# Performance work log

Hardware: AMD Instinct MI355X
Metric: run time of the kernel (lower is better)

## Reference

```python
import jax, jax.numpy as jnp
import numpy as np

B, N, K, F, L, H, ZMAX = 16, 1024, 16, 128, 4, 128, 100


def setup_inputs() -> dict:
    key = jax.random.key(0)
    ks = jax.random.split(key, 12)
    cell = jnp.eye(3, dtype=jnp.float32)[None] * 8.0 + 0.05 * jax.random.normal(ks[0], (B, 3, 3), dtype=jnp.float32)
    x = jax.random.uniform(ks[1], (B, N, 3), dtype=jnp.float32)
    z = jax.random.randint(ks[2], (B, N), 0, ZMAX)
    struct_size = jnp.full((B,), N, dtype=jnp.int32)
    emb = 0.02 * jax.random.normal(ks[3], (ZMAX, F), dtype=jnp.float32)
    din = 2 * F + 1
    W1 = jax.random.normal(ks[4], (L, din, F), dtype=jnp.float32) / np.sqrt(din)
    b1 = jnp.zeros((L, F), dtype=jnp.float32)
    W2 = jax.random.normal(ks[5], (L, F, F), dtype=jnp.float32) / np.sqrt(F)
    b2 = jnp.zeros((L, F), dtype=jnp.float32)
    A1 = jax.random.normal(ks[6], (din, H), dtype=jnp.float32) / np.sqrt(din)
    a1 = jnp.zeros((H,), dtype=jnp.float32)
    A2 = jax.random.normal(ks[7], (H, 1), dtype=jnp.float32) / np.sqrt(H)
    a2 = jnp.zeros((1,), dtype=jnp.float32)
    return {"cell": cell, "x": x, "z": z, "struct_size": struct_size, "emb": emb,
            "W1": W1, "b1": b1, "W2": W2, "b2": b2, "A1": A1, "a1": a1, "A2": A2, "a2": a2}


def _periodic_knn(cell, frac, k):
    # frac: [B,N,3] fractional coords, cell: [B,3,3] lattice rows.
    b, n, _ = frac.shape
    g = jnp.arange(-1, 2, dtype=frac.dtype)
    shifts = jnp.stack(jnp.meshgrid(g, g, g, indexing="ij"), -1).reshape(-1, 3)  # [27,3]
    rel = frac[:, None, :, :] - frac[:, :, None, :]  # rel[b,i,j] = frac_j - frac_i, [B,N,N,3]

    def body(carry, si):
        bd2, bsi = carry
        s, i = si
        cart = jnp.einsum("bijd,bde->bije", rel + s, cell)
        d2 = jnp.sum(cart * cart, axis=-1)
        upd = d2 < bd2
        return (jnp.where(upd, d2, bd2), jnp.where(upd, i, bsi)), None

    init = (jnp.full((b, n, n), 1e30, dtype=frac.dtype), jnp.zeros((b, n, n), dtype=jnp.int32))
    (d2min, simin), _ = jax.lax.scan(body, init, (shifts, jnp.arange(27, dtype=jnp.int32)))
    eye = jnp.eye(n, dtype=bool)
    d2min = jnp.where(eye[None], 1e30, d2min)  # exclude self (zero-shift) edges
    _, idx = jax.lax.top_k(-d2min, k)  # [B,N,k] neighbor indices
    sid = jnp.take_along_axis(simin, idx, axis=2)  # best image shift per edge
    svec = shifts[sid]  # [B,N,k,3]
    frac_j = jax.vmap(lambda f, i: f[i])(frac, idx)  # [B,N,k,3]
    vec = jnp.einsum("bnkd,bde->bnke", frac_j - frac[:, :, None, :] + svec, cell)
    d = jnp.sqrt(jnp.maximum(jnp.sum(vec * vec, axis=-1), 1e-12))  # [B,N,k]
    return idx, vec, d


def _edge_feat(h, idx, d):
    hj = jax.vmap(lambda hb, ib: hb[ib])(h, idx)  # [B,N,k,F]
    hi = jnp.broadcast_to(h[:, :, None, :], hj.shape)
    return jnp.concatenate([hi, hj, d[..., None]], axis=-1)  # [B,N,k,2F+1]


def reference(cell, x, z, struct_size, emb, W1, b1, W2, b2, A1, a1, A2, a2):
    frac = jnp.mod(x, 1.0)
    idx, vec, d = _periodic_knn(cell, frac, K)
    h = emb[z]  # [B,N,F]
    for l in range(W1.shape[0]):
        feat = _edge_feat(h, idx, d)
        m = jax.nn.silu(feat @ W1[l] + b1[l]) @ W2[l] + b2[l]  # [B,N,k,F]
        h = h + jnp.mean(m, axis=2)
    feat = _edge_feat(h, idx, d)
    w = jax.nn.silu(feat @ A1 + a1) @ A2 + a2  # [B,N,k,1]
    delta_cart = jnp.sum(w * vec, axis=2)  # [B,N,3]
    delta_frac = jnp.einsum("bnd,bde->bne", delta_cart, jnp.linalg.inv(cell))
    return x + delta_frac
```

## Files before the change

### kernel.cpp

```cpp
#include <hip/hip_runtime.h>

#define B_ 16
#define N_ 1024
#define K_ 16
#define F_ 128
#define L_ 4
#define DIN_ 257

typedef __bf16 bf16x8 __attribute__((ext_vector_type(8)));
typedef float f32x4 __attribute__((ext_vector_type(4)));

__device__ __forceinline__ float silu_f(float x) {
    return x / (1.0f + __expf(-x));
}

__device__ __forceinline__ unsigned short f2bf_bits(float f) {
    unsigned u = __builtin_bit_cast(unsigned, f);
    return (unsigned short)((u + 0x7FFFu + ((u >> 16) & 1u)) >> 16);
}

__global__ __launch_bounds__(256) void k_embed(const int* __restrict__ z,
                                               const float* __restrict__ emb,
                                               float* __restrict__ h,
                                               unsigned short* __restrict__ hbf) {
    int t = blockIdx.x * 256 + threadIdx.x;
    int node = t >> 5;
    int f4 = (t & 31) << 2;
    if (node >= B_ * N_) return;
    int zi = z[node];
    float4 v = *reinterpret_cast<const float4*>(&emb[zi * F_ + f4]);
    *reinterpret_cast<float4*>(&h[node * F_ + f4]) = v;
    ushort4 pk;
    pk.x = f2bf_bits(v.x); pk.y = f2bf_bits(v.y);
    pk.z = f2bf_bits(v.z); pk.w = f2bf_bits(v.w);
    *reinterpret_cast<ushort4*>(&hbf[node * F_ + f4]) = pk;
}

__global__ __launch_bounds__(256) void k_wconv(const float* __restrict__ W1,
                                               const float* __restrict__ W2,
                                               const float* __restrict__ A1,
                                               unsigned short* __restrict__ Wt1,
                                               unsigned short* __restrict__ Wt2,
                                               unsigned short* __restrict__ At1) {
    int id = blockIdx.x * 256 + threadIdx.x;
    if (id < L_ * 256 * 128) {
        int k = id & 127, n = (id >> 7) & 255, l = id >> 15;
        float v = (n < 128) ? W1[(size_t)l * DIN_ * F_ + (size_t)k * F_ + n]
                            : W1[(size_t)l * DIN_ * F_ + (size_t)(128 + k) * F_ + (n - 128)];
        Wt1[id] = f2bf_bits(v);
        return;
    }
    id -= L_ * 256 * 128;
    if (id < L_ * 128 * 128) {
        int k = id & 127, n = (id >> 7) & 127, l = id >> 14;
        Wt2[id] = f2bf_bits(W2[(size_t)l * F_ * F_ + (size_t)k * F_ + n]);
        return;
    }
    id -= L_ * 128 * 128;
    if (id < 256 * 128) {
        int k = id & 127, n = id >> 7;
        float v = (n < 128) ? A1[(size_t)k * 128 + n]
                            : A1[(size_t)(128 + k) * 128 + (n - 128)];
        At1[id] = f2bf_bits(v);
    }
}

__global__ __launch_bounds__(256) void k_knn(const float* __restrict__ x,
                                             const float* __restrict__ cell,
                                             int* __restrict__ idx_o,
                                             float* __restrict__ vec_o,
                                             float* __restrict__ d_o) {
    __shared__ float fr[N_ * 3];
    int b = blockIdx.x >> 8;
    int ib = (blockIdx.x & 255) << 2;
    const float* xb = x + b * N_ * 3;
    for (int u = threadIdx.x; u < N_ * 3; u += 256) {
        float xv = xb[u];
        fr[u] = xv - floorf(xv);
    }
    __syncthreads();
    int wave = threadIdx.x >> 6;
    int lane = threadIdx.x & 63;
    int i = ib + wave;

    const float* cb = cell + b * 9;
    float c00 = cb[0], c01 = cb[1], c02 = cb[2];
    float c10 = cb[3], c11 = cb[4], c12 = cb[5];
    float c20 = cb[6], c21 = cb[7], c22 = cb[8];
    float fi0 = fr[i * 3 + 0], fi1 = fr[i * 3 + 1], fi2 = fr[i * 3 + 2];

    unsigned long long k[16];
#pragma unroll
    for (int t = 0; t < 16; ++t) {
        int j = t * 64 + lane;
        float r0 = fr[j * 3 + 0] - fi0;
        float r1 = fr[j * 3 + 1] - fi1;
        float r2 = fr[j * 3 + 2] - fi2;
        float s0f = (r0 > 0.f) ? -1.f : 0.f;
        float s1f = (r1 > 0.f) ? -1.f : 0.f;
        float s2f = (r2 > 0.f) ? -1.f : 0.f;
        int sid_base = ((r0 > 0.f) ? 0 : 9) + ((r1 > 0.f) ? 0 : 3) + ((r2 > 0.f) ? 0 : 1);
        float rx0 = r0 + s0f, rx1 = r0 + (s0f + 1.0f);
        float ry0 = r1 + s1f, ry1 = r1 + (s1f + 1.0f);
        float rz0 = r2 + s2f, rz1 = r2 + (s2f + 1.0f);
        float best = 3e38f;
        int bsid = 0;
#pragma unroll
        for (int cbo = 0; cbo < 8; ++cbo) {
            float rs0 = (cbo & 4) ? rx1 : rx0;
            float rs1 = (cbo & 2) ? ry1 : ry0;
            float rs2 = (cbo & 1) ? rz1 : rz0;
            float cx = fmaf(rs2, c20, fmaf(rs1, c10, rs0 * c00));
            float cy = fmaf(rs2, c21, fmaf(rs1, c11, rs0 * c01));
            float cz = fmaf(rs2, c22, fmaf(rs1, c12, rs0 * c02));
            float d2 = fmaf(cz, cz, fmaf(cy, cy, cx * cx));
            int sid = sid_base + ((cbo >> 2) & 1) * 9 + ((cbo >> 1) & 1) * 3 + (cbo & 1);
            if (d2 < best) { best = d2; bsid = sid; }
        }
        if (j == i) best = 3e38f;
        unsigned db = __builtin_bit_cast(unsigned, best);
        k[t] = ((unsigned long long)db << 32) | (unsigned)((j << 5) | bsid);
    }

#define CE_(a, b)                                              \
    {                                                          \
        unsigned long long x_ = k[a], y_ = k[b];               \
        bool s_ = y_ < x_;                                     \
        k[a] = s_ ? y_ : x_;                                   \
        k[b] = s_ ? x_ : y_;                                   \
    }
    CE_(0,1) CE_(2,3) CE_(4,5) CE_(6,7) CE_(8,9) CE_(10,11) CE_(12,13) CE_(14,15)
    CE_(0,2) CE_(1,3) CE_(4,6) CE_(5,7) CE_(8,10) CE_(9,11) CE_(12,14) CE_(13,15)
    CE_(1,2) CE_(5,6) CE_(9,10) CE_(13,14)
    CE_(0,4) CE_(1,5) CE_(2,6) CE_(3,7) CE_(8,12) CE_(9,13) CE_(10,14) CE_(11,15)
    CE_(2,4) CE_(3,5) CE_(10,12) CE_(11,13)
    CE_(1,2) CE_(3,4) CE_(5,6) CE_(9,10) CE_(11,12) CE_(13,14)
    CE_(0,8) CE_(1,9) CE_(2,10) CE_(3,11) CE_(4,12) CE_(5,13) CE_(6,14) CE_(7,15)
    CE_(4,8) CE_(5,9) CE_(6,10) CE_(7,11)
    CE_(2,4) CE_(3,5) CE_(6,8) CE_(7,9) CE_(10,12) CE_(11,13)
    CE_(1,2) CE_(3,4) CE_(5,6) CE_(7,8) CE_(9,10) CE_(11,12) CE_(13,14)
#undef CE_

    unsigned long long sel = 0;
    for (int r = 0; r < 16; ++r) {
        unsigned long long m = k[0];
#pragma unroll
        for (int off = 32; off >= 1; off >>= 1) {
            unsigned long long o = __shfl_xor(m, off);
            if (o < m) m = o;
        }
        if (k[0] == m) {
#pragma unroll
            for (int t = 0; t < 15; ++t) k[t] = k[t + 1];
            k[15] = ~0ull;
        }
        if (lane == r) sel = m;
    }

    if (lane < 16) {
        unsigned pk = (unsigned)sel;
        int j = pk >> 5, sid = pk & 31;
        int s0 = sid / 9 - 1, s1 = (sid / 3) % 3 - 1, s2 = sid % 3 - 1;
        float rs0 = (fr[j * 3 + 0] - fi0) + (float)s0;
        float rs1 = (fr[j * 3 + 1] - fi1) + (float)s1;
        float rs2 = (fr[j * 3 + 2] - fi2) + (float)s2;
        float vx = fmaf(rs2, c20, fmaf(rs1, c10, rs0 * c00));
        float vy = fmaf(rs2, c21, fmaf(rs1, c11, rs0 * c01));
        float vz = fmaf(rs2, c22, fmaf(rs1, c12, rs0 * c02));
        float d2 = fmaf(vz, vz, fmaf(vy, vy, vx * vx));
        float dd = sqrtf(fmaxf(d2, 1e-12f));
        int node = b * N_ + i;
        int eo = node * K_ + lane;
        idx_o[eo] = j;
        d_o[eo] = dd;
        vec_o[eo * 3 + 0] = vx;
        vec_o[eo * 3 + 1] = vy;
        vec_o[eo * 3 + 2] = vz;
    }
}

template <int LOG_NT>
__global__ __launch_bounds__(256) void k_wgemm(const unsigned short* __restrict__ A,
                                               const unsigned short* __restrict__ Bt,
                                               float* __restrict__ C, int ldc) {
    constexpr int NT = 1 << LOG_NT;
    int wave = threadIdx.x >> 6, lane = threadIdx.x & 63;
    int tile = blockIdx.x * 4 + wave;
    int mt = tile >> LOG_NT, nt = tile & (NT - 1);
    int fr16 = lane & 15, ko = lane >> 4;
    const unsigned short* Ap = A + (size_t)(mt * 32 + fr16) * 128 + ko * 8;
    const unsigned short* Bp = Bt + (size_t)(nt * 32 + fr16) * 128 + ko * 8;

    bf16x8 a0[4], a1[4], b0[4], b1[4];
#pragma unroll
    for (int ks = 0; ks < 4; ++ks) {
        a0[ks] = *reinterpret_cast<const bf16x8*>(Ap + ks * 32);
        a1[ks] = *reinterpret_cast<const bf16x8*>(Ap + 16 * 128 + ks * 32);
        b0[ks] = *reinterpret_cast<const bf16x8*>(Bp + ks * 32);
        b1[ks] = *reinterpret_cast<const bf16x8*>(Bp + 16 * 128 + ks * 32);
    }
    f32x4 acc00 = {0.f, 0.f, 0.f, 0.f}, acc01 = acc00, acc10 = acc00, acc11 = acc00;
#pragma unroll
    for (int ks = 0; ks < 4; ++ks) {
        acc00 = __builtin_amdgcn_mfma_f32_16x16x32_bf16(a0[ks], b0[ks], acc00, 0, 0, 0);
        acc01 = __builtin_amdgcn_mfma_f32_16x16x32_bf16(a0[ks], b1[ks], acc01, 0, 0, 0);
        acc10 = __builtin_amdgcn_mfma_f32_16x16x32_bf16(a1[ks], b0[ks], acc10, 0, 0, 0);
        acc11 = __builtin_amdgcn_mfma_f32_16x16x32_bf16(a1[ks], b1[ks], acc11, 0, 0, 0);
    }
    int mrow = mt * 32 + ko * 4;
    int cbase = nt * 32 + fr16;
#define EPI_(FM, FN, ACC)                                                    \
    {                                                                        \
        int cc = cbase + FN * 16;                                            \
        _Pragma("unroll") for (int r = 0; r < 4; ++r) {                      \
            int row = mrow + FM * 16 + r;                                    \
            C[(size_t)row * ldc + cc] = ACC[r];                              \
        }                                                                    \
    }
    EPI_(0, 0, acc00) EPI_(0, 1, acc01) EPI_(1, 0, acc10) EPI_(1, 1, acc11)
#undef EPI_
}

__global__ __launch_bounds__(256) void k_layer(const float* __restrict__ UVin,
                                               const int* __restrict__ idx,
                                               const float* __restrict__ nd,
                                               const float* __restrict__ w1d,
                                               const float* __restrict__ b1l,
                                               const unsigned short* __restrict__ W2t,
                                               const float* __restrict__ b2l,
                                               float* __restrict__ h,
                                               const unsigned short* __restrict__ W1n,
                                               float* __restrict__ UVout) {
    __shared__ unsigned short svl[32][136];
    __shared__ unsigned short hbl[32][136];
    __shared__ int ilds[512];
    __shared__ float dlds[512];
    int tid = threadIdx.x;
    int gb = blockIdx.x;
    int batch = (gb & 7) + 8 * (gb >> 8);
    int ib = (gb >> 3) & 31;
    int node0 = batch * N_ + ib * 32;
    int bbase = batch * N_;

    ilds[tid] = idx[node0 * K_ + tid];
    ilds[tid + 256] = idx[node0 * K_ + tid + 256];
    dlds[tid] = nd[node0 * K_ + tid];
    dlds[tid + 256] = nd[node0 * K_ + tid + 256];
    __syncthreads();

#pragma unroll
    for (int it = 0; it < 2; ++it) {
        int tsk = it * 256 + tid;
        int gn = tsk >> 4, fc = tsk & 15, f0 = fc << 3;
        int node = node0 + gn;
        float u[8], wd[8], bb[8], acc[8];
#pragma unroll
        for (int q = 0; q < 8; q += 4) {
            float4 t = *reinterpret_cast<const float4*>(&UVin[(size_t)node * 256 + f0 + q]);
            u[q] = t.x; u[q + 1] = t.y; u[q + 2] = t.z; u[q + 3] = t.w;
            float4 t2 = *reinterpret_cast<const float4*>(&w1d[f0 + q]);
            wd[q] = t2.x; wd[q + 1] = t2.y; wd[q + 2] = t2.z; wd[q + 3] = t2.w;
            float4 t3 = *reinterpret_cast<const float4*>(&b1l[f0 + q]);
            bb[q] = t3.x; bb[q + 1] = t3.y; bb[q + 2] = t3.z; bb[q + 3] = t3.w;
        }
#pragma unroll
        for (int q = 0; q < 8; ++q) acc[q] = 0.f;
        for (int e = 0; e < K_; ++e) {
            int j = ilds[gn * K_ + e];
            float dd = dlds[gn * K_ + e];
            const float* vp = &UVin[(size_t)(bbase + j) * 256 + 128 + f0];
#pragma unroll
            for (int q = 0; q < 8; q += 4) {
                float4 t = *reinterpret_cast<const float4*>(&vp[q]);
                float v4[4] = {t.x, t.y, t.z, t.w};
#pragma unroll
                for (int w = 0; w < 4; ++w) {
                    float pre = u[q + w] + v4[w] + fmaf(dd, wd[q + w], bb[q + w]);
                    acc[q + w] += silu_f(pre);
                }
            }
        }
        const float inv_k = 1.0f / (float)K_;
        unsigned ow[4];
#pragma unroll
        for (int q = 0; q < 4; ++q)
            ow[q] = (unsigned)f2bf_bits(acc[2 * q] * inv_k) |
                    ((unsigned)f2bf_bits(acc[2 * q + 1] * inv_k) << 16);
        *reinterpret_cast<int4*>(&svl[gn][f0]) = make_int4(ow[0], ow[1], ow[2], ow[3]);
    }
    __syncthreads();

    int wave = tid >> 6, lane = tid & 63;
    int fr16 = lane & 15, ko = lane >> 4;

    {
        const unsigned short* Bp = W2t + (size_t)(wave * 32 + fr16) * 128 + ko * 8;
        bf16x8 a0[4], a1[4], b0[4], b1f[4];
#pragma unroll
        for (int ks = 0; ks < 4; ++ks) {
            a0[ks] = *reinterpret_cast<const bf16x8*>(&svl[fr16][ks * 32 + ko * 8]);
            a1[ks] = *reinterpret_cast<const bf16x8*>(&svl[fr16 + 16][ks * 32 + ko * 8]);
            b0[ks] = *reinterpret_cast<const bf16x8*>(Bp + ks * 32);
            b1f[ks] = *reinterpret_cast<const bf16x8*>(Bp + 16 * 128 + ks * 32);
        }
        f32x4 acc00 = {0.f, 0.f, 0.f, 0.f}, acc01 = acc00, acc10 = acc00, acc11 = acc00;
#pragma unroll
        for (int ks = 0; ks < 4; ++ks) {
            acc00 = __builtin_amdgcn_mfma_f32_16x16x32_bf16(a0[ks], b0[ks], acc00, 0, 0, 0);
            acc01 = __builtin_amdgcn_mfma_f32_16x16x32_bf16(a0[ks], b1f[ks], acc01, 0, 0, 0);
            acc10 = __builtin_amdgcn_mfma_f32_16x16x32_bf16(a1[ks], b0[ks], acc10, 0, 0, 0);
            acc11 = __builtin_amdgcn_mfma_f32_16x16x32_bf16(a1[ks], b1f[ks], acc11, 0, 0, 0);
        }
        int mrow = ko * 4;
        int cb0 = wave * 32 + fr16;
#define EPI2_(FM, FN, ACC)                                                     \
    {                                                                          \
        int col = cb0 + FN * 16;                                               \
        float bv = b2l[col];                                                   \
        _Pragma("unroll") for (int r = 0; r < 4; ++r) {                        \
            int row = mrow + FM * 16 + r;                                      \
            int grow = node0 + row;                                            \
            float val = ACC[r] + bv + h[(size_t)grow * 128 + col];             \
            h[(size_t)grow * 128 + col] = val;                                 \
            hbl[row][col] = f2bf_bits(val);                                    \
        }                                                                      \
    }
        EPI2_(0, 0, acc00) EPI2_(0, 1, acc01) EPI2_(1, 0, acc10) EPI2_(1, 1, acc11)
#undef EPI2_
    }
    __syncthreads();

#pragma unroll
    for (int half = 0; half < 2; ++half) {
        int nt = wave + half * 4;
        const unsigned short* Bp = W1n + (size_t)(nt * 32 + fr16) * 128 + ko * 8;
        bf16x8 a0[4], a1[4], b0[4], b1f[4];
#pragma unroll
        for (int ks = 0; ks < 4; ++ks) {
            a0[ks] = *reinterpret_cast<const bf16x8*>(&hbl[fr16][ks * 32 + ko * 8]);
            a1[ks] = *reinterpret_cast<const bf16x8*>(&hbl[fr16 + 16][ks * 32 + ko * 8]);
            b0[ks] = *reinterpret_cast<const bf16x8*>(Bp + ks * 32);
            b1f[ks] = *reinterpret_cast<const bf16x8*>(Bp + 16 * 128 + ks * 32);
        }
        f32x4 acc00 = {0.f, 0.f, 0.f, 0.f}, acc01 = acc00, acc10 = acc00, acc11 = acc00;
#pragma unroll
        for (int ks = 0; ks < 4; ++ks) {
            acc00 = __builtin_amdgcn_mfma_f32_16x16x32_bf16(a0[ks], b0[ks], acc00, 0, 0, 0);
            acc01 = __builtin_amdgcn_mfma_f32_16x16x32_bf16(a0[ks], b1f[ks], acc01, 0, 0, 0);
            acc10 = __builtin_amdgcn_mfma_f32_16x16x32_bf16(a1[ks], b0[ks], acc10, 0, 0, 0);
            acc11 = __builtin_amdgcn_mfma_f32_16x16x32_bf16(a1[ks], b1f[ks], acc11, 0, 0, 0);
        }
        int mrow = ko * 4;
        int cb0 = nt * 32 + fr16;
#define EPI1_(FM, FN, ACC)                                                     \
    {                                                                          \
        int col = cb0 + FN * 16;                                               \
        _Pragma("unroll") for (int r = 0; r < 4; ++r) {                        \
            int row = mrow + FM * 16 + r;                                      \
            UVout[(size_t)(node0 + row) * 256 + col] = ACC[r];                 \
        }                                                                      \
    }
        EPI1_(0, 0, acc00) EPI1_(0, 1, acc01) EPI1_(1, 0, acc10) EPI1_(1, 1, acc11)
#undef EPI1_
    }
}

__global__ __launch_bounds__(256) void k_final(const float* __restrict__ P,
                                               const int* __restrict__ idx,
                                               const float* __restrict__ nd,
                                               const float* __restrict__ nvec,
                                               const float* __restrict__ A1d,
                                               const float* __restrict__ a1v,
                                               const float* __restrict__ A2v,
                                               const float* __restrict__ a2v,
                                               const float* __restrict__ x,
                                               const float* __restrict__ cell,
                                               float* __restrict__ out) {
    __shared__ float plds[16][256];
    __shared__ float wlds[16][17];
    __shared__ float dclds[16][3];
    int gb = blockIdx.x;
    int batch = (gb & 7) + 8 * (gb >> 9);
    int ib = (gb >> 3) & 63;
    int node0 = batch * N_ + ib * 16;
    int g = threadIdx.x >> 4, fc = threadIdx.x & 15;
    int node = node0 + g;
    int b = node >> 10;
    int f0 = fc * 8;
    float pa[8], ad[8], aa[8], a2r[8];
#pragma unroll
    for (int q = 0; q < 8; q += 4) {
        float4 t = *reinterpret_cast<const float4*>(&P[(size_t)node * 256 + f0 + q]);
        pa[q] = t.x; pa[q + 1] = t.y; pa[q + 2] = t.z; pa[q + 3] = t.w;
        float4 t2 = *reinterpret_cast<const float4*>(&A1d[f0 + q]);
        ad[q] = t2.x; ad[q + 1] = t2.y; ad[q + 2] = t2.z; ad[q + 3] = t2.w;
        float4 t3 = *reinterpret_cast<const float4*>(&a1v[f0 + q]);
        aa[q] = t3.x; aa[q + 1] = t3.y; aa[q + 2] = t3.z; aa[q + 3] = t3.w;
        float4 t4 = *reinterpret_cast<const float4*>(&A2v[f0 + q]);
        a2r[q] = t4.x; a2r[q + 1] = t4.y; a2r[q + 2] = t4.z; a2r[q + 3] = t4.w;
    }
    int ebase = node * K_;
    for (int e = 0; e < K_; ++e) {
        int j = idx[ebase + e];
        float dd = nd[ebase + e];
        const float* vp = &P[(size_t)(b * N_ + j) * 256 + 128 + f0];
        float part = 0.f;
#pragma unroll
        for (int q = 0; q < 8; q += 4) {
            float4 t = *reinterpret_cast<const float4*>(&vp[q]);
            float v4[4] = {t.x, t.y, t.z, t.w};
#pragma unroll
            for (int w = 0; w < 4; ++w) {
                float pre = pa[q + w] + v4[w] + fmaf(dd, ad[q + w], aa[q + w]);
                part = fmaf(silu_f(pre), a2r[q + w], part);
            }
        }
        plds[e][(g << 4) | fc] = part;
    }
    __syncthreads();
    {
        int g2 = threadIdx.x >> 4, e2 = threadIdx.x & 15;
        float w = a2v[0];
#pragma unroll
        for (int f2 = 0; f2 < 16; ++f2) w += plds[e2][(g2 << 4) | f2];
        wlds[g2][e2] = w;
    }
    __syncthreads();
    if (threadIdx.x < 48) {
        int gg = threadIdx.x & 15, c = threadIdx.x >> 4;
        int noded = node0 + gg;
        float dc = 0.f;
#pragma unroll
        for (int e = 0; e < K_; ++e)
            dc = fmaf(wlds[gg][e], nvec[(size_t)(noded * K_ + e) * 3 + c], dc);
        dclds[gg][c] = dc;
    }
    __syncthreads();
    if (threadIdx.x < 48) {
        int gg = threadIdx.x & 15, c = threadIdx.x >> 4;
        int noded = node0 + gg;
        int bb2 = noded >> 10;
        const float* cb = cell + bb2 * 9;
        float c00 = cb[0], c01 = cb[1], c02 = cb[2];
        float c10 = cb[3], c11 = cb[4], c12 = cb[5];
        float c20 = cb[6], c21 = cb[7], c22 = cb[8];
        float det = c00 * (c11 * c22 - c12 * c21) - c01 * (c10 * c22 - c12 * c20) +
                    c02 * (c10 * c21 - c11 * c20);
        float rdet = 1.0f / det;
        float i0c, i1c, i2c;
        if (c == 0) {
            i0c = (c11 * c22 - c12 * c21) * rdet;
            i1c = -(c10 * c22 - c12 * c20) * rdet;
            i2c = (c10 * c21 - c11 * c20) * rdet;
        } else if (c == 1) {
            i0c = -(c01 * c22 - c02 * c21) * rdet;
            i1c = (c00 * c22 - c02 * c20) * rdet;
            i2c = -(c00 * c21 - c01 * c20) * rdet;
        } else {
            i0c = (c01 * c12 - c02 * c11) * rdet;
            i1c = -(c00 * c12 - c02 * c10) * rdet;
            i2c = (c00 * c11 - c01 * c10) * rdet;
        }
        float df = dclds[gg][0] * i0c + dclds[gg][1] * i1c + dclds[gg][2] * i2c;
        out[(size_t)noded * 3 + c] = x[(size_t)noded * 3 + c] + df;
    }
}

extern "C" void kernel_launch(void* const* d_in, const int* in_sizes, int n_in,
                              void* d_out, int out_size, void* d_ws, size_t ws_size,
                              hipStream_t stream) {
    (void)in_sizes; (void)n_in; (void)out_size; (void)ws_size;
    const float* cell = (const float*)d_in[0];
    const float* x    = (const float*)d_in[1];
    const int*   z    = (const int*)d_in[2];
    const float* emb  = (const float*)d_in[4];
    const float* W1   = (const float*)d_in[5];
    const float* b1   = (const float*)d_in[6];
    const float* W2   = (const float*)d_in[7];
    const float* b2   = (const float*)d_in[8];
    const float* A1   = (const float*)d_in[9];
    const float* a1   = (const float*)d_in[10];
    const float* A2   = (const float*)d_in[11];
    const float* a2   = (const float*)d_in[12];
    float* out = (float*)d_out;

    char* ws = (char*)d_ws;
    size_t off = 0;
    auto alloc = [&](size_t bytes) {
        void* p = ws + off;
        off = (off + bytes + 255) & ~(size_t)255;
        return p;
    };
    int* idx    = (int*)alloc((size_t)B_ * N_ * K_ * 4);
    float* nd   = (float*)alloc((size_t)B_ * N_ * K_ * 4);
    float* nvec = (float*)alloc((size_t)B_ * N_ * K_ * 3 * 4);
    float* h0   = (float*)alloc((size_t)B_ * N_ * F_ * 4);
    float* uv0  = (float*)alloc((size_t)B_ * N_ * 256 * 4);
    float* uv1  = (float*)alloc((size_t)B_ * N_ * 256 * 4);
    unsigned short* hbf = (unsigned short*)alloc((size_t)B_ * N_ * F_ * 2);
    unsigned short* Wt1 = (unsigned short*)alloc((size_t)L_ * 256 * 128 * 2);
    unsigned short* Wt2 = (unsigned short*)alloc((size_t)L_ * 128 * 128 * 2);
    unsigned short* At1 = (unsigned short*)alloc((size_t)256 * 128 * 2);

    int conv_total = L_ * 256 * 128 + L_ * 128 * 128 + 256 * 128;
    k_wconv<<<(conv_total + 255) / 256, 256, 0, stream>>>(W1, W2, A1, Wt1, Wt2, At1);
    k_embed<<<2048, 256, 0, stream>>>(z, emb, h0, hbf);
    k_knn<<<4096, 256, 0, stream>>>(x, cell, idx, nvec, nd);

    k_wgemm<3><<<1024, 256, 0, stream>>>(hbf, Wt1, uv0, 256);

    for (int l = 0; l < L_; ++l) {
        const float* uin = (l & 1) ? uv1 : uv0;
        float* uout = (l & 1) ? uv0 : uv1;
        const unsigned short* W1next = (l < 3) ? (Wt1 + (size_t)(l + 1) * 256 * 128) : At1;
        k_layer<<<512, 256, 0, stream>>>(uin, idx, nd,
                                         W1 + (size_t)l * DIN_ * F_ + 256 * F_, b1 + l * F_,
                                         Wt2 + (size_t)l * 128 * 128, b2 + l * F_, h0,
                                         W1next, uout);
    }
    k_final<<<1024, 256, 0, stream>>>(uv0, idx, nd, nvec, A1 + 256 * F_, a1, A2, a2, x, cell,
                                      out);
}
```

Before: 270.2 us.

## Merge prep kernels, fuse first GEMM into kNN, halve layer tile size

Weight conversion and embedding are merged into one prep kernel. The kNN kernel now handles 16 nodes per block (4 per wave) and ends with the first h@W1 GEMM tile, which removes a separate launch. The layer kernel is rewritten to 16 nodes per block with 1024 blocks, meant to raise occupancy and parallelism. The cost is that each MFMA tile reuses its weights across half as many rows, and the kNN blocks loop serially over four query rows each.

```diff
diff --git a/kernel.cpp b/kernel.cpp
--- a/kernel.cpp
+++ b/kernel.cpp
@@ -19,108 +19,116 @@
     return (unsigned short)((u + 0x7FFFu + ((u >> 16) & 1u)) >> 16);
 }
 
-__global__ __launch_bounds__(256) void k_embed(const int* __restrict__ z,
-                                               const float* __restrict__ emb,
-                                               float* __restrict__ h,
-                                               unsigned short* __restrict__ hbf) {
-    int t = blockIdx.x * 256 + threadIdx.x;
-    int node = t >> 5;
-    int f4 = (t & 31) << 2;
-    if (node >= B_ * N_) return;
-    int zi = z[node];
-    float4 v = *reinterpret_cast<const float4*>(&emb[zi * F_ + f4]);
-    *reinterpret_cast<float4*>(&h[node * F_ + f4]) = v;
-    ushort4 pk;
-    pk.x = f2bf_bits(v.x); pk.y = f2bf_bits(v.y);
-    pk.z = f2bf_bits(v.z); pk.w = f2bf_bits(v.w);
-    *reinterpret_cast<ushort4*>(&hbf[node * F_ + f4]) = pk;
-}
-
-__global__ __launch_bounds__(256) void k_wconv(const float* __restrict__ W1,
-                                               const float* __restrict__ W2,
-                                               const float* __restrict__ A1,
-                                               unsigned short* __restrict__ Wt1,
-                                               unsigned short* __restrict__ Wt2,
-                                               unsigned short* __restrict__ At1) {
-    int id = blockIdx.x * 256 + threadIdx.x;
+__global__ __launch_bounds__(256) void k_prep(const int* __restrict__ z,
+                                              const float* __restrict__ emb,
+                                              const float* __restrict__ W1,
+                                              const float* __restrict__ W2,
+                                              const float* __restrict__ A1,
+                                              float* __restrict__ h,
+                                              unsigned short* __restrict__ hbf,
+                                              unsigned short* __restrict__ Wt1,
+                                              unsigned short* __restrict__ Wt2,
+                                              unsigned short* __restrict__ At1) {
+    int gid = blockIdx.x * 256 + threadIdx.x;
+    int id = gid;
     if (id < L_ * 256 * 128) {
         int k = id & 127, n = (id >> 7) & 255, l = id >> 15;
         float v = (n < 128) ? W1[(size_t)l * DIN_ * F_ + (size_t)k * F_ + n]
                             : W1[(size_t)l * DIN_ * F_ + (size_t)(128 + k) * F_ + (n - 128)];
         Wt1[id] = f2bf_bits(v);
-        return;
-    }
-    id -= L_ * 256 * 128;
-    if (id < L_ * 128 * 128) {
-        int k = id & 127, n = (id >> 7) & 127, l = id >> 14;
-        Wt2[id] = f2bf_bits(W2[(size_t)l * F_ * F_ + (size_t)k * F_ + n]);
-        return;
-    }
-    id -= L_ * 128 * 128;
-    if (id < 256 * 128) {
-        int k = id & 127, n = id >> 7;
-        float v = (n < 128) ? A1[(size_t)k * 128 + n]
-                            : A1[(size_t)(128 + k) * 128 + (n - 128)];
-        At1[id] = f2bf_bits(v);
-    }
-}
-
-__global__ __launch_bounds__(256) void k_knn(const float* __restrict__ x,
-                                             const float* __restrict__ cell,
-                                             int* __restrict__ idx_o,
-                                             float* __restrict__ vec_o,
-                                             float* __restrict__ d_o) {
+    } else {
+        int id2 = id - L_ * 256 * 128;
+        if (id2 < L_ * 128 * 128) {
+            int k = id2 & 127, n = (id2 >> 7) & 127, l = id2 >> 14;
+            Wt2[id2] = f2bf_bits(W2[(size_t)l * F_ * F_ + (size_t)k * F_ + n]);
+        } else {
+            int id3 = id2 - L_ * 128 * 128;
+            if (id3 < 256 * 128) {
+                int k = id3 & 127, n = id3 >> 7;
+                float v = (n < 128) ? A1[(size_t)k * 128 + n]
+                                    : A1[(size_t)(128 + k) * 128 + (n - 128)];
+                At1[id3] = f2bf_bits(v);
+            }
+        }
+    }
+    {
+        int t = gid;
+        int node = t >> 5;
+        int f4 = (t & 31) << 2;
+        int zi = z[node];
+        float4 v = *reinterpret_cast<const float4*>(&emb[zi * F_ + f4]);
+        *reinterpret_cast<float4*>(&h[node * F_ + f4]) = v;
+        ushort4 pk;
+        pk.x = f2bf_bits(v.x); pk.y = f2bf_bits(v.y);
+        pk.z = f2bf_bits(v.z); pk.w = f2bf_bits(v.w);
+        *reinterpret_cast<ushort4*>(&hbf[node * F_ + f4]) = pk;
+    }
+}
+
+__global__ __launch_bounds__(256) void k_knng(const float* __restrict__ x,
+                                              const float* __restrict__ cell,
+                                              int* __restrict__ idx_o,
+                                              float* __restrict__ vec_o,
+                                              float* __restrict__ d_o,
+                                              const unsigned short* __restrict__ hbf,
+                                              const unsigned short* __restrict__ Wt1,
+                                              float* __restrict__ uv0) {
     __shared__ float fr[N_ * 3];
-    int b = blockIdx.x >> 8;
-    int ib = (blockIdx.x & 255) << 2;
-    const float* xb = x + b * N_ * 3;
-    for (int u = threadIdx.x; u < N_ * 3; u += 256) {
+    int tid = threadIdx.x;
+    int gb = blockIdx.x;
+    int batch = gb >> 6;
+    int ib = gb & 63;
+    const float* xb = x + batch * N_ * 3;
+    for (int u = tid; u < N_ * 3; u += 256) {
         float xv = xb[u];
         fr[u] = xv - floorf(xv);
     }
     __syncthreads();
-    int wave = threadIdx.x >> 6;
-    int lane = threadIdx.x & 63;
-    int i = ib + wave;
-
-    const float* cb = cell + b * 9;
+    int wave = tid >> 6;
+    int lane = tid & 63;
+    int fr16 = lane & 15, ko = lane >> 4;
+
+    const float* cb = cell + batch * 9;
     float c00 = cb[0], c01 = cb[1], c02 = cb[2];
     float c10 = cb[3], c11 = cb[4], c12 = cb[5];
     float c20 = cb[6], c21 = cb[7], c22 = cb[8];
-    float fi0 = fr[i * 3 + 0], fi1 = fr[i * 3 + 1], fi2 = fr[i * 3 + 2];
-
-    unsigned long long k[16];
-#pragma unroll
-    for (int t = 0; t < 16; ++t) {
-        int j = t * 64 + lane;
-        float r0 = fr[j * 3 + 0] - fi0;
-        float r1 = fr[j * 3 + 1] - fi1;
-        float r2 = fr[j * 3 + 2] - fi2;
-        float s0f = (r0 > 0.f) ? -1.f : 0.f;
-        float s1f = (r1 > 0.f) ? -1.f : 0.f;
-        float s2f = (r2 > 0.f) ? -1.f : 0.f;
-        int sid_base = ((r0 > 0.f) ? 0 : 9) + ((r1 > 0.f) ? 0 : 3) + ((r2 > 0.f) ? 0 : 1);
-        float rx0 = r0 + s0f, rx1 = r0 + (s0f + 1.0f);
-        float ry0 = r1 + s1f, ry1 = r1 + (s1f + 1.0f);
-        float rz0 = r2 + s2f, rz1 = r2 + (s2f + 1.0f);
-        float best = 3e38f;
-        int bsid = 0;
-#pragma unroll
-        for (int cbo = 0; cbo < 8; ++cbo) {
-            float rs0 = (cbo & 4) ? rx1 : rx0;
-            float rs1 = (cbo & 2) ? ry1 : ry0;
-            float rs2 = (cbo & 1) ? rz1 : rz0;
-            float cx = fmaf(rs2, c20, fmaf(rs1, c10, rs0 * c00));
-            float cy = fmaf(rs2, c21, fmaf(rs1, c11, rs0 * c01));
-            float cz = fmaf(rs2, c22, fmaf(rs1, c12, rs0 * c02));
-            float d2 = fmaf(cz, cz, fmaf(cy, cy, cx * cx));
-            int sid = sid_base + ((cbo >> 2) & 1) * 9 + ((cbo >> 1) & 1) * 3 + (cbo & 1);
-            if (d2 < best) { best = d2; bsid = sid; }
-        }
-        if (j == i) best = 3e38f;
-        unsigned db = __builtin_bit_cast(unsigned, best);
-        k[t] = ((unsigned long long)db << 32) | (unsigned)((j << 5) | bsid);
-    }
+
+    for (int r4 = 0; r4 < 4; ++r4) {
+        int i = ib * 16 + wave * 4 + r4;
+        float fi0 = fr[i * 3 + 0], fi1 = fr[i * 3 + 1], fi2 = fr[i * 3 + 2];
+
+        unsigned long long k[16];
+#pragma unroll
+        for (int t = 0; t < 16; ++t) {
+            int j = t * 64 + lane;
+            float r0 = fr[j * 3 + 0] - fi0;
+            float r1 = fr[j * 3 + 1] - fi1;
+            float r2 = fr[j * 3 + 2] - fi2;
+            float s0f = (r0 > 0.f) ? -1.f : 0.f;
+            float s1f = (r1 > 0.f) ? -1.f : 0.f;
+            float s2f = (r2 > 0.f) ? -1.f : 0.f;
+            int sid_base = ((r0 > 0.f) ? 0 : 9) + ((r1 > 0.f) ? 0 : 3) + ((r2 > 0.f) ? 0 : 1);
+            float rx0 = r0 + s0f, rx1 = r0 + (s0f + 1.0f);
+            float ry0 = r1 + s1f, ry1 = r1 + (s1f + 1.0f);
+            float rz0 = r2 + s2f, rz1 = r2 + (s2f + 1.0f);
+            float best = 3e38f;
+            int bsid = 0;
+#pragma unroll
+            for (int cbo = 0; cbo < 8; ++cbo) {
+                float rs0 = (cbo & 4) ? rx1 : rx0;
+                float rs1 = (cbo & 2) ? ry1 : ry0;
+                float rs2 = (cbo & 1) ? rz1 : rz0;
+                float cx = fmaf(rs2, c20, fmaf(rs1, c10, rs0 * c00));
+                float cy = fmaf(rs2, c21, fmaf(rs1, c11, rs0 * c01));
+                float cz = fmaf(rs2, c22, fmaf(rs1, c12, rs0 * c02));
+                float d2 = fmaf(cz, cz, fmaf(cy, cy, cx * cx));
+                int sid = sid_base + ((cbo >> 2) & 1) * 9 + ((cbo >> 1) & 1) * 3 + (cbo & 1);
+                if (d2 < best) { best = d2; bsid = sid; }
+            }
+            if (j == i) best = 3e38f;
+            unsigned db = __builtin_bit_cast(unsigned, best);
+            k[t] = ((unsigned long long)db << 32) | (unsigned)((j << 5) | bsid);
+        }
 
 #define CE_(a, b)                                              \
     {                                                          \
@@ -129,129 +137,121 @@
         k[a] = s_ ? y_ : x_;                                   \
         k[b] = s_ ? x_ : y_;                                   \
     }
-    CE_(0,1) CE_(2,3) CE_(4,5) CE_(6,7) CE_(8,9) CE_(10,11) CE_(12,13) CE_(14,15)
-    CE_(0,2) CE_(1,3) CE_(4,6) CE_(5,7) CE_(8,10) CE_(9,11) CE_(12,14) CE_(13,15)
-    CE_(1,2) CE_(5,6) CE_(9,10) CE_(13,14)
-    CE_(0,4) CE_(1,5) CE_(2,6) CE_(3,7) CE_(8,12) CE_(9,13) CE_(10,14) CE_(11,15)
-    CE_(2,4) CE_(3,5) CE_(10,12) CE_(11,13)
-    CE_(1,2) CE_(3,4) CE_(5,6) CE_(9,10) CE_(11,12) CE_(13,14)
-    CE_(0,8) CE_(1,9) CE_(2,10) CE_(3,11) CE_(4,12) CE_(5,13) CE_(6,14) CE_(7,15)
-    CE_(4,8) CE_(5,9) CE_(6,10) CE_(7,11)
-    CE_(2,4) CE_(3,5) CE_(6,8) CE_(7,9) CE_(10,12) CE_(11,13)
-    CE_(1,2) CE_(3,4) CE_(5,6) CE_(7,8) CE_(9,10) CE_(11,12) CE_(13,14)
+        CE_(0,1) CE_(2,3) CE_(4,5) CE_(6,7) CE_(8,9) CE_(10,11) CE_(12,13) CE_(14,15)
+        CE_(0,2) CE_(1,3) CE_(4,6) CE_(5,7) CE_(8,10) CE_(9,11) CE_(12,14) CE_(13,15)
+        CE_(1,2) CE_(5,6) CE_(9,10) CE_(13,14)
+        CE_(0,4) CE_(1,5) CE_(2,6) CE_(3,7) CE_(8,12) CE_(9,13) CE_(10,14) CE_(11,15)
+        CE_(2,4) CE_(3,5) CE_(10,12) CE_(11,13)
+        CE_(1,2) CE_(3,4) CE_(5,6) CE_(9,10) CE_(11,12) CE_(13,14)
+        CE_(0,8) CE_(1,9) CE_(2,10) CE_(3,11) CE_(4,12) CE_(5,13) CE_(6,14) CE_(7,15)
+        CE_(4,8) CE_(5,9) CE_(6,10) CE_(7,11)
+        CE_(2,4) CE_(3,5) CE_(6,8) CE_(7,9) CE_(10,12) CE_(11,13)
+        CE_(1,2) CE_(3,4) CE_(5,6) CE_(7,8) CE_(9,10) CE_(11,12) CE_(13,14)
 #undef CE_
 
-    unsigned long long sel = 0;
-    for (int r = 0; r < 16; ++r) {
-        unsigned long long m = k[0];
-#pragma unroll
-        for (int off = 32; off >= 1; off >>= 1) {
-            unsigned long long o = __shfl_xor(m, off);
-            if (o < m) m = o;
-        }
-        if (k[0] == m) {
-#pragma unroll
-            for (int t = 0; t < 15; ++t) k[t] = k[t + 1];
-            k[15] = ~0ull;
-        }
-        if (lane == r) sel = m;
-    }
-
-    if (lane < 16) {
-        unsigned pk = (unsigned)sel;
-        int j = pk >> 5, sid = pk & 31;
-        int s0 = sid / 9 - 1, s1 = (sid / 3) % 3 - 1, s2 = sid % 3 - 1;
-        float rs0 = (fr[j * 3 + 0] - fi0) + (float)s0;
-        float rs1 = (fr[j * 3 + 1] - fi1) + (float)s1;
-        float rs2 = (fr[j * 3 + 2] - fi2) + (float)s2;
-        float vx = fmaf(rs2, c20, fmaf(rs1, c10, rs0 * c00));
-        float vy = fmaf(rs2, c21, fmaf(rs1, c11, rs0 * c01));
-        float vz = fmaf(rs2, c22, fmaf(rs1, c12, rs0 * c02));
-        float d2 = fmaf(vz, vz, fmaf(vy, vy, vx * vx));
-        float dd = sqrtf(fmaxf(d2, 1e-12f));
-        int node = b * N_ + i;
-        int eo = node * K_ + lane;
-        idx_o[eo] = j;
-        d_o[eo] = dd;
-        vec_o[eo * 3 + 0] = vx;
-        vec_o[eo * 3 + 1] = vy;
-        vec_o[eo * 3 + 2] = vz;
-    }
-}
-
-template <int LOG_NT>
-__global__ __launch_bounds__(256) void k_wgemm(const unsigned short* __restrict__ A,
-                                               const unsigned short* __restrict__ Bt,
-                                               float* __restrict__ C, int ldc) {
-    constexpr int NT = 1 << LOG_NT;
-    int wave = threadIdx.x >> 6, lane = threadIdx.x & 63;
-    int tile = blockIdx.x * 4 + wave;
-    int mt = tile >> LOG_NT, nt = tile & (NT - 1);
-    int fr16 = lane & 15, ko = lane >> 4;
-    const unsigned short* Ap = A + (size_t)(mt * 32 + fr16) * 128 + ko * 8;
-    const unsigned short* Bp = Bt + (size_t)(nt * 32 + fr16) * 128 + ko * 8;
-
-    bf16x8 a0[4], a1[4], b0[4], b1[4];
-#pragma unroll
-    for (int ks = 0; ks < 4; ++ks) {
-        a0[ks] = *reinterpret_cast<const bf16x8*>(Ap + ks * 32);
-        a1[ks] = *reinterpret_cast<const bf16x8*>(Ap + 16 * 128 + ks * 32);
-        b0[ks] = *reinterpret_cast<const bf16x8*>(Bp + ks * 32);
-        b1[ks] = *reinterpret_cast<const bf16x8*>(Bp + 16 * 128 + ks * 32);
-    }
-    f32x4 acc00 = {0.f, 0.f, 0.f, 0.f}, acc01 = acc00, acc10 = acc00, acc11 = acc00;
-#pragma unroll
-    for (int ks = 0; ks < 4; ++ks) {
-        acc00 = __builtin_amdgcn_mfma_f32_16x16x32_bf16(a0[ks], b0[ks], acc00, 0, 0, 0);
-        acc01 = __builtin_amdgcn_mfma_f32_16x16x32_bf16(a0[ks], b1[ks], acc01, 0, 0, 0);
-        acc10 = __builtin_amdgcn_mfma_f32_16x16x32_bf16(a1[ks], b0[ks], acc10, 0, 0, 0);
-        acc11 = __builtin_amdgcn_mfma_f32_16x16x32_bf16(a1[ks], b1[ks], acc11, 0, 0, 0);
-    }
-    int mrow = mt * 32 + ko * 4;
-    int cbase = nt * 32 + fr16;
+        unsigned long long sel = 0;
+        for (int r = 0; r < 16; ++r) {
+            unsigned long long m = k[0];
+#pragma unroll
+            for (int off = 32; off >= 1; off >>= 1) {
+                unsigned long long o = __shfl_xor(m, off);
+                if (o < m) m = o;
+            }
+            if (k[0] == m) {
+#pragma unroll
+                for (int t = 0; t < 15; ++t) k[t] = k[t + 1];
+                k[15] = ~0ull;
+            }
+            if (lane == r) sel = m;
+        }
+
+        if (lane < 16) {
+            unsigned pk = (unsigned)sel;
+            int j = pk >> 5, sid = pk & 31;
+            int s0 = sid / 9 - 1, s1 = (sid / 3) % 3 - 1, s2 = sid % 3 - 1;
+            float rs0 = (fr[j * 3 + 0] - fi0) + (float)s0;
+            float rs1 = (fr[j * 3 + 1] - fi1) + (float)s1;
+            float rs2 = (fr[j * 3 + 2] - fi2) + (float)s2;
+            float vx = fmaf(rs2, c20, fmaf(rs1, c10, rs0 * c00));
+            float vy = fmaf(rs2, c21, fmaf(rs1, c11, rs0 * c01));
+            float vz = fmaf(rs2, c22, fmaf(rs1, c12, rs0 * c02));
+            float d2 = fmaf(vz, vz, fmaf(vy, vy, vx * vx));
+            float dd = sqrtf(fmaxf(d2, 1e-12f));
+            int node = batch * N_ + i;
+            int eo = node * K_ + lane;
+            idx_o[eo] = j;
+            d_o[eo] = dd;
+            vec_o[eo * 3 + 0] = vx;
+            vec_o[eo * 3 + 1] = vy;
+            vec_o[eo * 3 + 2] = vz;
+        }
+    }
+
+    {
+        int t = gb * 4 + wave;
+        int mt = t >> 3, nt = t & 7;
+        const unsigned short* Ap = hbf + (size_t)(mt * 32 + fr16) * 128 + ko * 8;
+        const unsigned short* Bp = Wt1 + (size_t)(nt * 32 + fr16) * 128 + ko * 8;
+        bf16x8 a0[4], a1v_[4], b0[4], b1v_[4];
+#pragma unroll
+        for (int ks = 0; ks < 4; ++ks) {
+            a0[ks] = *reinterpret_cast<const bf16x8*>(Ap + ks * 32);
+            a1v_[ks] = *reinterpret_cast<const bf16x8*>(Ap + 16 * 128 + ks * 32);
+            b0[ks] = *reinterpret_cast<const bf16x8*>(Bp + ks * 32);
+            b1v_[ks] = *reinterpret_cast<const bf16x8*>(Bp + 16 * 128 + ks * 32);
+        }
+        f32x4 acc00 = {0.f, 0.f, 0.f, 0.f}, acc01 = acc00, acc10 = acc00, acc11 = acc00;
+#pragma unroll
+        for (int ks = 0; ks < 4; ++ks) {
+            acc00 = __builtin_amdgcn_mfma_f32_16x16x32_bf16(a0[ks], b0[ks], acc00, 0, 0, 0);
+            acc01 = __builtin_amdgcn_mfma_f32_16x16x32_bf16(a0[ks], b1v_[ks], acc01, 0, 0, 0);
+            acc10 = __builtin_amdgcn_mfma_f32_16x16x32_bf16(a1v_[ks], b0[ks], acc10, 0, 0, 0);
+            acc11 = __builtin_amdgcn_mfma_f32_16x16x32_bf16(a1v_[ks], b1v_[ks], acc11, 0, 0, 0);
+        }
+        int mrow = mt * 32 + ko * 4;
+        int cbase = nt * 32 + fr16;
 #define EPI_(FM, FN, ACC)                                                    \
     {                                                                        \
         int cc = cbase + FN * 16;                                            \
         _Pragma("unroll") for (int r = 0; r < 4; ++r) {                      \
             int row = mrow + FM * 16 + r;                                    \
-            C[(size_t)row * ldc + cc] = ACC[r];                              \
+            uv0[(size_t)row * 256 + cc] = ACC[r];                            \
         }                                                                    \
     }
-    EPI_(0, 0, acc00) EPI_(0, 1, acc01) EPI_(1, 0, acc10) EPI_(1, 1, acc11)
+        EPI_(0, 0, acc00) EPI_(0, 1, acc01) EPI_(1, 0, acc10) EPI_(1, 1, acc11)
 #undef EPI_
-}
-
-__global__ __launch_bounds__(256) void k_layer(const float* __restrict__ UVin,
-                                               const int* __restrict__ idx,
-                                               const float* __restrict__ nd,
-                                               const float* __restrict__ w1d,
-                                               const float* __restrict__ b1l,
-                                               const unsigned short* __restrict__ W2t,
-                                               const float* __restrict__ b2l,
-                                               float* __restrict__ h,
-                                               const unsigned short* __restrict__ W1n,
-                                               float* __restrict__ UVout) {
-    __shared__ unsigned short svl[32][136];
-    __shared__ unsigned short hbl[32][136];
-    __shared__ int ilds[512];
-    __shared__ float dlds[512];
+    }
+}
+
+__global__ __launch_bounds__(256) void k_layer16(const float* __restrict__ UVin,
+                                                 const int* __restrict__ idx,
+                                                 const float* __restrict__ nd,
+                                                 const float* __restrict__ w1d,
+                                                 const float* __restrict__ b1l,
+                                                 const unsigned short* __restrict__ W2t,
+                                                 const float* __restrict__ b2l,
+                                                 float* __restrict__ h,
+                                                 const unsigned short* __restrict__ W1n,
+                                                 float* __restrict__ UVout) {
+    __shared__ unsigned short svl[16][136];
+    __shared__ unsigned short hbl[16][136];
+    __shared__ int ilds[256];
+    __shared__ float dlds[256];
     int tid = threadIdx.x;
     int gb = blockIdx.x;
-    int batch = (gb & 7) + 8 * (gb >> 8);
-    int ib = (gb >> 3) & 31;
-    int node0 = batch * N_ + ib * 32;
+    int batch = (gb & 7) + 8 * (gb >> 9);
+    int ib = (gb >> 3) & 63;
+    int node0 = batch * N_ + ib * 16;
     int bbase = batch * N_;
+    int wave = tid >> 6, lane = tid & 63;
+    int fr16 = lane & 15, ko = lane >> 4;
 
     ilds[tid] = idx[node0 * K_ + tid];
-    ilds[tid + 256] = idx[node0 * K_ + tid + 256];
     dlds[tid] = nd[node0 * K_ + tid];
-    dlds[tid + 256] = nd[node0 * K_ + tid + 256];
-    __syncthreads();
-
-#pragma unroll
-    for (int it = 0; it < 2; ++it) {
-        int tsk = it * 256 + tid;
-        int gn = tsk >> 4, fc = tsk & 15, f0 = fc << 3;
+    __syncthreads();
+
+    {
+        int gn = tid >> 4, fc = tid & 15, f0 = fc << 3;
         int node = node0 + gn;
         float u[8], wd[8], bb[8], acc[8];
 #pragma unroll
@@ -290,77 +290,66 @@
     }
     __syncthreads();
 
-    int wave = tid >> 6, lane = tid & 63;
-    int fr16 = lane & 15, ko = lane >> 4;
-
     {
         const unsigned short* Bp = W2t + (size_t)(wave * 32 + fr16) * 128 + ko * 8;
-        bf16x8 a0[4], a1[4], b0[4], b1f[4];
+        bf16x8 a0[4], b0[4], b1f[4];
 #pragma unroll
         for (int ks = 0; ks < 4; ++ks) {
             a0[ks] = *reinterpret_cast<const bf16x8*>(&svl[fr16][ks * 32 + ko * 8]);
-            a1[ks] = *reinterpret_cast<const bf16x8*>(&svl[fr16 + 16][ks * 32 + ko * 8]);
             b0[ks] = *reinterpret_cast<const bf16x8*>(Bp + ks * 32);
             b1f[ks] = *reinterpret_cast<const bf16x8*>(Bp + 16 * 128 + ks * 32);
         }
-        f32x4 acc00 = {0.f, 0.f, 0.f, 0.f}, acc01 = acc00, acc10 = acc00, acc11 = acc00;
+        f32x4 acc00 = {0.f, 0.f, 0.f, 0.f}, acc01 = acc00;
 #pragma unroll
         for (int ks = 0; ks < 4; ++ks) {
             acc00 = __builtin_amdgcn_mfma_f32_16x16x32_bf16(a0[ks], b0[ks], acc00, 0, 0, 0);
             acc01 = __builtin_amdgcn_mfma_f32_16x16x32_bf16(a0[ks], b1f[ks], acc01, 0, 0, 0);
-            acc10 = __builtin_amdgcn_mfma_f32_16x16x32_bf16(a1[ks], b0[ks], acc10, 0, 0, 0);
-            acc11 = __builtin_amdgcn_mfma_f32_16x16x32_bf16(a1[ks], b1f[ks], acc11, 0, 0, 0);
-        }
-        int mrow = ko * 4;
+        }
         int cb0 = wave * 32 + fr16;
-#define EPI2_(FM, FN, ACC)                                                     \
+#define EPI2_(FN, ACC)                                                         \
     {                                                                          \
         int col = cb0 + FN * 16;                                               \
         float bv = b2l[col];                                                   \
         _Pragma("unroll") for (int r = 0; r < 4; ++r) {                        \
-            int row = mrow + FM * 16 + r;                                      \
+            int row = ko * 4 + r;                                              \
             int grow = node0 + row;                                            \
             float val = ACC[r] + bv + h[(size_t)grow * 128 + col];             \
             h[(size_t)grow * 128 + col] = val;                                 \
             hbl[row][col] = f2bf_bits(val);                                    \
         }                                                                      \
     }
-        EPI2_(0, 0, acc00) EPI2_(0, 1, acc01) EPI2_(1, 0, acc10) EPI2_(1, 1, acc11)
+        EPI2_(0, acc00) EPI2_(1, acc01)
 #undef EPI2_
     }
     __syncthreads();
 
 #pragma unroll
     for (int half = 0; half < 2; ++half) {
-        int nt = wave + half * 4;
-        const unsigned short* Bp = W1n + (size_t)(nt * 32 + fr16) * 128 + ko * 8;
-        bf16x8 a0[4], a1[4], b0[4], b1f[4];
+        int nt2 = wave + half * 4;
+        const unsigned short* Bp = W1n + (size_t)(nt2 * 32 + fr16) * 128 + ko * 8;
+        bf16x8 a0[4], b0[4], b1f[4];
 #pragma unroll
         for (int ks = 0; ks < 4; ++ks) {
             a0[ks] = *reinterpret_cast<const bf16x8*>(&hbl[fr16][ks * 32 + ko * 8]);
-            a1[ks] = *reinterpret_cast<const bf16x8*>(&hbl[fr16 + 16][ks * 32 + ko * 8]);
             b0[ks] = *reinterpret_cast<const bf16x8*>(Bp + ks * 32);
             b1f[ks] = *reinterpret_cast<const bf16x8*>(Bp + 16 * 128 + ks * 32);
         }
-        f32x4 acc00 = {0.f, 0.f, 0.f, 0.f}, acc01 = acc00, acc10 = acc00, acc11 = acc00;
+        f32x4 acc00 = {0.f, 0.f, 0.f, 0.f}, acc01 = acc00;
 #pragma unroll
         for (int ks = 0; ks < 4; ++ks) {
             acc00 = __builtin_amdgcn_mfma_f32_16x16x32_bf16(a0[ks], b0[ks], acc00, 0, 0, 0);
             acc01 = __builtin_amdgcn_mfma_f32_16x16x32_bf16(a0[ks], b1f[ks], acc01, 0, 0, 0);
-            acc10 = __builtin_amdgcn_mfma_f32_16x16x32_bf16(a1[ks], b0[ks], acc10, 0, 0, 0);
-            acc11 = __builtin_amdgcn_mfma_f32_16x16x32_bf16(a1[ks], b1f[ks], acc11, 0, 0, 0);
-        }
-        int mrow = ko * 4;
-        int cb0 = nt * 32 + fr16;
-#define EPI1_(FM, FN, ACC)                                                     \
+        }
+        int cb0 = nt2 * 32 + fr16;
+#define EPI1_(FN, ACC)                                                         \
     {                                                                          \
         int col = cb0 + FN * 16;                                               \
         _Pragma("unroll") for (int r = 0; r < 4; ++r) {                        \
-            int row = mrow + FM * 16 + r;                                      \
+            int row = ko * 4 + r;                                              \
             UVout[(size_t)(node0 + row) * 256 + col] = ACC[r];                 \
         }                                                                      \
     }
-        EPI1_(0, 0, acc00) EPI1_(0, 1, acc01) EPI1_(1, 0, acc10) EPI1_(1, 1, acc11)
+        EPI1_(0, acc00) EPI1_(1, acc01)
 #undef EPI1_
     }
 }
@@ -502,21 +491,17 @@
     unsigned short* Wt2 = (unsigned short*)alloc((size_t)L_ * 128 * 128 * 2);
     unsigned short* At1 = (unsigned short*)alloc((size_t)256 * 128 * 2);
 
-    int conv_total = L_ * 256 * 128 + L_ * 128 * 128 + 256 * 128;
-    k_wconv<<<(conv_total + 255) / 256, 256, 0, stream>>>(W1, W2, A1, Wt1, Wt2, At1);
-    k_embed<<<2048, 256, 0, stream>>>(z, emb, h0, hbf);
-    k_knn<<<4096, 256, 0, stream>>>(x, cell, idx, nvec, nd);
-
-    k_wgemm<3><<<1024, 256, 0, stream>>>(hbf, Wt1, uv0, 256);
+    k_prep<<<2048, 256, 0, stream>>>(z, emb, W1, W2, A1, h0, hbf, Wt1, Wt2, At1);
+    k_knng<<<1024, 256, 0, stream>>>(x, cell, idx, nvec, nd, hbf, Wt1, uv0);
 
     for (int l = 0; l < L_; ++l) {
         const float* uin = (l & 1) ? uv1 : uv0;
         float* uout = (l & 1) ? uv0 : uv1;
         const unsigned short* W1next = (l < 3) ? (Wt1 + (size_t)(l + 1) * 256 * 128) : At1;
-        k_layer<<<512, 256, 0, stream>>>(uin, idx, nd,
-                                         W1 + (size_t)l * DIN_ * F_ + 256 * F_, b1 + l * F_,
-                                         Wt2 + (size_t)l * 128 * 128, b2 + l * F_, h0,
-                                         W1next, uout);
+        k_layer16<<<1024, 256, 0, stream>>>(uin, idx, nd,
+                                            W1 + (size_t)l * DIN_ * F_ + 256 * F_,
+                                            b1 + l * F_, Wt2 + (size_t)l * 128 * 128,
+                                            b2 + l * F_, h0, W1next, uout);
     }
     k_final<<<1024, 256, 0, stream>>>(uv0, idx, nd, nvec, A1 + 256 * F_, a1, A2, a2, x, cell,
                                       out);
```

After: 273.5 us. Within noise of the previous version (+1.2%).
